# Kernel optimization log

Measured on AMD Instinct MI355X. Metric: run time of the kernel, lower is better.

Reference implementation:

```python
import jax, jax.numpy as jnp
from jax import lax
import numpy as np

V = 4096                 # variants per batch
NUM_READ_FEATURES = 24
NUM_INFO_FEATURES = 10
REF_LEN = 25             # ref sequence length (one-hot over ACGT)
CONV_C = 32
KERN = 3
READ_E = 128
INFO_E = 64
SEQ_E = 64
EMB = READ_E + INFO_E + SEQ_E   # 256, matches hstack of read/info/seq embeddings
FFN = 512                # self_attention_hidden_dimension
NUM_BLOCKS = 2           # num_self_attention_layers
AGG_H = 256
AGG_OUT = 128
WEIGHT_RANGE = 0.2


def _init_params(key):
    ks = iter(jax.random.split(key, 40))
    def lin(din, dout):
        w = jax.random.normal(next(ks), (din, dout), jnp.float32) / np.float32(np.sqrt(din))
        return w, jnp.zeros((dout,), jnp.float32)
    p = {}
    p['read_w1'], p['read_b1'] = lin(NUM_READ_FEATURES, READ_E)
    p['read_w2'], p['read_b2'] = lin(READ_E, READ_E)
    p['info_w1'], p['info_b1'] = lin(NUM_INFO_FEATURES, INFO_E)
    p['info_w2'], p['info_b2'] = lin(INFO_E, INFO_E)
    p['conv_w'] = jax.random.normal(next(ks), (CONV_C, 4, KERN), jnp.float32) / np.float32(np.sqrt(4 * KERN))
    p['conv_b'] = jnp.zeros((CONV_C,), jnp.float32)
    flat = CONV_C * (REF_LEN - KERN + 1)
    p['seq_w'], p['seq_b'] = lin(flat, SEQ_E)
    p['blk_w1'] = jax.random.normal(next(ks), (NUM_BLOCKS, EMB, FFN), jnp.float32) / np.float32(np.sqrt(EMB))
    p['blk_b1'] = jnp.zeros((NUM_BLOCKS, FFN), jnp.float32)
    p['blk_wg'] = jax.random.normal(next(ks), (NUM_BLOCKS, EMB, FFN), jnp.float32) / np.float32(np.sqrt(EMB))
    p['blk_bg'] = jnp.zeros((NUM_BLOCKS, FFN), jnp.float32)
    p['blk_w2'] = jax.random.normal(next(ks), (NUM_BLOCKS, FFN, EMB), jnp.float32) / np.float32(np.sqrt(FFN))
    p['blk_b2'] = jnp.zeros((NUM_BLOCKS, EMB), jnp.float32)
    p['agg_w1'], p['agg_b1'] = lin(EMB, AGG_H)
    p['agg_w2'], p['agg_b2'] = lin(AGG_H, AGG_OUT)
    return p


def setup_inputs() -> dict:
    rng = np.random.default_rng(0)
    ref_counts_np = rng.integers(5, 45, size=V)
    alt_counts_np = rng.integers(2, 23, size=V)
    total_ref = int(ref_counts_np.sum())
    total_alt = int(alt_counts_np.sum())
    key = jax.random.key(0)
    k1, k2, k3, kp = jax.random.split(key, 4)
    reads_2d = jax.random.normal(k1, (total_ref + total_alt, NUM_READ_FEATURES), jnp.float32)
    info_2d = jax.random.normal(k2, (V, NUM_INFO_FEATURES), jnp.float32)
    base_idx = rng.integers(0, 4, size=(V, REF_LEN))
    ref_seq_oh = jnp.asarray(np.eye(4, dtype=np.float32)[base_idx].transpose(0, 2, 1))  # [V,4,L]
    alt_u = jax.random.uniform(k3, (total_alt,), jnp.float32)  # replaces torch.rand for alt weights
    inp = {
        'reads_2d': reads_2d, 'info_2d': info_2d, 'ref_seq_oh': ref_seq_oh, 'alt_u': alt_u,
        'ref_counts': jnp.asarray(ref_counts_np, jnp.int32),
        'alt_counts': jnp.asarray(alt_counts_np, jnp.int32),
    }
    inp.update(_init_params(kp))
    return inp


def _mlp2(x, w1, b1, w2, b2):
    return jax.nn.relu(x @ w1 + b1) @ w2 + b2


def _forward(reads_2d, info_2d, ref_seq_oh, alt_u,
             read_w1, read_b1, read_w2, read_b2,
             info_w1, info_b1, info_w2, info_b2,
             conv_w, conv_b, seq_w, seq_b,
             blk_w1, blk_b1, blk_wg, blk_bg, blk_w2, blk_b2,
             agg_w1, agg_b1, agg_w2, agg_b2,
             ref_counts, alt_counts):
    total_alt = alt_u.shape[0]
    total_ref = reads_2d.shape[0] - total_alt
    # per-read and per-variant embeddings
    read_re = _mlp2(reads_2d, read_w1, read_b1, read_w2, read_b2)          # [R, READ_E]
    info_ve = _mlp2(info_2d, info_w1, info_b1, info_w2, info_b2)           # [V, INFO_E]
    conv = lax.conv_general_dilated(ref_seq_oh, conv_w, window_strides=(1,), padding='VALID',
                                    dimension_numbers=('NCH', 'OIH', 'NCH'))
    conv = jax.nn.relu(conv + conv_b[None, :, None])                       # [V, C, L-K+1]
    seq_ve = conv.reshape(conv.shape[0], -1) @ seq_w + seq_b               # [V, SEQ_E]
    info_seq_ve = jnp.concatenate([info_ve, seq_ve], axis=1)               # [V, INFO_E+SEQ_E]
    # ragged broadcast: variant-level rows repeated per read (repeat_interleave)
    ref_ids = jnp.repeat(jnp.arange(V), ref_counts, total_repeat_length=total_ref)
    alt_ids = jnp.repeat(jnp.arange(V), alt_counts, total_repeat_length=total_alt)
    ref_x = jnp.concatenate([read_re[:total_ref], info_seq_ve[ref_ids]], axis=1)   # [total_ref, EMB]
    alt_x = jnp.concatenate([read_re[total_ref:], info_seq_ve[alt_ids]], axis=1)   # [total_alt, EMB]
    ref_cf = ref_counts.astype(ref_x.dtype)[:, None]
    alt_cf = alt_counts.astype(alt_x.dtype)[:, None]
    # gated ref/alt encoder: per-read MLP cross-gated by the other set's segment mean
    for i in range(NUM_BLOCKS):
        ref_mean = jax.ops.segment_sum(ref_x, ref_ids, num_segments=V) / ref_cf
        alt_mean = jax.ops.segment_sum(alt_x, alt_ids, num_segments=V) / alt_cf
        def blk(x, gate_src):
            h = jax.nn.relu(x @ blk_w1[i] + blk_b1[i]) * jax.nn.sigmoid(gate_src @ blk_wg[i] + blk_bg[i])
            return h @ blk_w2[i] + blk_b2[i]
        ref_x = ref_x + blk(ref_x, alt_mean[ref_ids])
        alt_x = alt_x + blk(alt_x, ref_mean[alt_ids])
    # normalized weighted segment sums over alt reads (utils.sums_over_rows)
    w_r = 1.0 + WEIGHT_RANGE * (1.0 - 2.0 * alt_u)                          # [total_alt]
    wt_sums_v = jax.ops.segment_sum(w_r, alt_ids, num_segments=V)           # [V]
    norm_w = w_r / wt_sums_v[alt_ids]
    alt_means_ve = jax.ops.segment_sum(alt_x * norm_w[:, None], alt_ids, num_segments=V)  # [V, EMB]
    return _mlp2(alt_means_ve, agg_w1, agg_b1, agg_w2, agg_b2)              # [V, AGG_OUT]


def reference(reads_2d, info_2d, ref_seq_oh, alt_u,
              read_w1, read_b1, read_w2, read_b2,
              info_w1, info_b1, info_w2, info_b2,
              conv_w, conv_b, seq_w, seq_b,
              blk_w1, blk_b1, blk_wg, blk_bg, blk_w2, blk_b2,
              agg_w1, agg_b1, agg_w2, agg_b2,
              ref_counts, alt_counts):
    return _forward(reads_2d, info_2d, ref_seq_oh, alt_u,
                    read_w1, read_b1, read_w2, read_b2,
                    info_w1, info_b1, info_w2, info_b2,
                    conv_w, conv_b, seq_w, seq_b,
                    blk_w1, blk_b1, blk_wg, blk_bg, blk_w2, blk_b2,
                    agg_w1, agg_b1, agg_w2, agg_b2,
                    ref_counts, alt_counts)
```

## Files before the change

### kernel.cpp

```cpp
#include <hip/hip_runtime.h>
#include <math.h>


typedef short short8 __attribute__((ext_vector_type(8)));
typedef __bf16 bf16x8 __attribute__((ext_vector_type(8)));
typedef float f32x4 __attribute__((ext_vector_type(4)));

__device__ inline unsigned short f2bf(float f) {
    unsigned u = __builtin_bit_cast(unsigned, f);
    u += 0x7fffu + ((u >> 16) & 1u);
    return (unsigned short)(u >> 16);
}
__device__ inline float bf2f(unsigned short u) {
    unsigned v = ((unsigned)u) << 16;
    return __builtin_bit_cast(float, v);
}

__device__ inline f32x4 mfma16(short8 a, short8 b, f32x4 c) {
    return __builtin_amdgcn_mfma_f32_16x16x32_bf16(
        __builtin_bit_cast(bf16x8, a), __builtin_bit_cast(bf16x8, b), c, 0, 0, 0);
}

__device__ inline int lds_idx(int row, int k, int Kp, int mask) {
    return row * Kp + (k ^ ((row & mask) << 3));
}

__global__ __launch_bounds__(256) void scan_fill(
        const int* __restrict__ cref, const int* __restrict__ calt,
        int* __restrict__ off_r, int* __restrict__ off_a,
        int* __restrict__ rid_r, int* __restrict__ rid_a, int V) {
    __shared__ int part[256];
    const int* cnt = blockIdx.x ? calt : cref;
    int* off = blockIdx.x ? off_a : off_r;
    int* rid = blockIdx.x ? rid_a : rid_r;
    int t = threadIdx.x;
    int items = (V + 255) >> 8;
    int base = t * items;
    int s = 0;
    for (int i = 0; i < items; i++) {
        int idx = base + i;
        if (idx < V) s += cnt[idx];
    }
    part[t] = s;
    __syncthreads();
    for (int d = 1; d < 256; d <<= 1) {
        int v = (t >= d) ? part[t - d] : 0;
        __syncthreads();
        part[t] += v;
        __syncthreads();
    }
    int run = (t == 0) ? 0 : part[t - 1];
    for (int i = 0; i < items; i++) {
        int idx = base + i;
        if (idx < V) {
            off[idx] = run;
            run += cnt[idx];
        }
    }
    if (t == 255) off[V] = part[255];
    __syncthreads();
    for (int v = t; v < V; v += 256) {
        int s0 = off[v], e0 = off[v + 1];
        for (int r = s0; r < e0; r++) rid[r] = v;
    }
}

__device__ inline void pack_one(const float* __restrict__ src,
                                unsigned short* __restrict__ dst, int i,
                                int Ksrc, int K, int N, int ctN) {
    int e = i & 7;
    int lane = (i >> 3) & 63;
    int li = lane & 15, lg = lane >> 4;
    int r = i >> 9;
    int ct = r % ctN;
    int r2 = r / ctN;
    int sN = K >> 5;
    int s = r2 % sN;
    int strip = r2 / sN;
    int n = strip * (ctN << 4) + (ct << 4) + li;
    int k = (s << 5) + (lg << 3) + e;
    dst[i] = (k < Ksrc) ? f2bf(src[(size_t)k * N + n]) : (unsigned short)0;
}

__global__ __launch_bounds__(256) void pack_all(
        const float* __restrict__ w1, const float* __restrict__ wg,
        const float* __restrict__ w2, const float* __restrict__ rw1,
        const float* __restrict__ rw2, const float* __restrict__ ag1,
        const float* __restrict__ ag2,
        unsigned short* W1p0, unsigned short* W1p1,
        unsigned short* Wgp0, unsigned short* Wgp1,
        unsigned short* W2p0, unsigned short* W2p1,
        unsigned short* RW1p, unsigned short* RW2p,
        unsigned short* AG1p, unsigned short* AG2p) {
    int idx = blockIdx.x * 256 + threadIdx.x;
    if (idx < 131072)       pack_one(w1,          W1p0, idx,          256, 256, 512, 4);
    else if (idx < 262144)  pack_one(w1 + 131072, W1p1, idx - 131072, 256, 256, 512, 4);
    else if (idx < 393216)  pack_one(wg,          Wgp0, idx - 262144, 256, 256, 512, 4);
    else if (idx < 524288)  pack_one(wg + 131072, Wgp1, idx - 393216, 256, 256, 512, 4);
    else if (idx < 655360)  pack_one(w2,          W2p0, idx - 524288, 512, 512, 256, 2);
    else if (idx < 786432)  pack_one(w2 + 131072, W2p1, idx - 655360, 512, 512, 256, 2);
    else if (idx < 790528)  pack_one(rw1,         RW1p, idx - 786432, 24, 32, 128, 1);
    else if (idx < 806912)  pack_one(rw2,         RW2p, idx - 790528, 128, 128, 128, 1);
    else if (idx < 872448)  pack_one(ag1,         AG1p, idx - 806912, 256, 256, 256, 4);
    else if (idx < 905216)  pack_one(ag2,         AG2p, idx - 872448, 256, 256, 128, 4);
}

template <int EPI>
__global__ __launch_bounds__(256, 4) void gemm_bf16(
        const unsigned short* __restrict__ A, const unsigned short* __restrict__ Bp,
        const float* __restrict__ bias, void* __restrict__ C0,
        int M, int K, int mask, int ldc) {
    extern __shared__ unsigned short As[];
    const int m0 = blockIdx.x * 64, n0 = blockIdx.y * 64;
    const int tid = threadIdx.x;
    const int kc = K >> 3;
    for (int i = tid; i < (kc << 6); i += 256) {
        int r = i / kc, k8 = (i - r * kc) << 3;
        short8 v = {0, 0, 0, 0, 0, 0, 0, 0};
        if (m0 + r < M) v = *(const short8*)(A + (size_t)(m0 + r) * K + k8);
        *(short8*)&As[lds_idx(r, k8, K, mask)] = v;
    }
    __syncthreads();
    const int wid = tid >> 6, lane = tid & 63;
    const int lr = lane & 15, lg = lane >> 4;
    f32x4 acc[4];
#pragma unroll
    for (int ct = 0; ct < 4; ++ct) acc[ct] = f32x4{0.f, 0.f, 0.f, 0.f};
    const unsigned short* Bb = Bp + (size_t)blockIdx.y * ((size_t)K << 6) + (lane << 3);
    const int nk = K >> 5;
    for (int s = 0; s < nk; ++s) {
        int k0 = (s << 5) + (lg << 3);
        short8 af = *(const short8*)&As[lds_idx((wid << 4) + lr, k0, K, mask)];
#pragma unroll
        for (int ct = 0; ct < 4; ++ct) {
            short8 bf = *(const short8*)(Bb + (s << 11) + (ct << 9));
            acc[ct] = mfma16(af, bf, acc[ct]);
        }
    }
#pragma unroll
    for (int ct = 0; ct < 4; ++ct) {
        int c = n0 + (ct << 4) + lr;
        float bb = bias[c];
#pragma unroll
        for (int q = 0; q < 4; ++q) {
            int rg = m0 + (wid << 4) + (lg << 2) + q;
            if (rg >= M) continue;
            float v = acc[ct][q] + bb;
            if (EPI == 0) {
                ((float*)C0)[(size_t)rg * ldc + c] = v;
            } else if (EPI == 1) {
                ((unsigned short*)C0)[(size_t)rg * ldc + c] = f2bf(fmaxf(v, 0.f));
            } else {
                ((unsigned short*)C0)[(size_t)rg * ldc + c] = f2bf(1.f / (1.f + __expf(-v)));
            }
        }
    }
}

__global__ __launch_bounds__(512) void read_mlp_fused(
        const float* __restrict__ reads,
        const unsigned short* __restrict__ RW1p, const unsigned short* __restrict__ RW2p,
        const float* __restrict__ rb1, const float* __restrict__ rb2,
        const uint4* __restrict__ isv4,
        const int* __restrict__ rid_r, const int* __restrict__ rid_a,
        unsigned short* __restrict__ xref, unsigned short* __restrict__ xalt,
        int R, int TR) {
    __shared__ unsigned short Xs[64 * 32];
    __shared__ unsigned short Hs[64 * 128];
    __shared__ int rid_s[64];
    const int m0 = blockIdx.x * 64;
    const int tid = threadIdx.x;
    if (tid < 64) {
        int g = m0 + tid;
        rid_s[tid] = (g < R) ? (g < TR ? rid_r[g] : rid_a[g - TR]) : 0;
    }
    if (tid < 256) {
        int r = tid >> 2, c8 = (tid & 3) << 3;
        short8 v = {0, 0, 0, 0, 0, 0, 0, 0};
        int g = m0 + r;
        if (g < R && c8 < 24) {
            const float* sp = reads + (size_t)g * 24 + c8;
#pragma unroll
            for (int e = 0; e < 8; e++) v[e] = (short)f2bf(sp[e]);
        }
        *(short8*)&Xs[lds_idx(r, c8, 32, 3)] = v;
    }
    __syncthreads();
    const int wid = tid >> 6, lane = tid & 63;
    const int li = lane & 15, lg = lane >> 4;
    f32x4 a1[4];
#pragma unroll
    for (int rt = 0; rt < 4; ++rt) a1[rt] = f32x4{0.f, 0.f, 0.f, 0.f};
    short8 bw1 = *(const short8*)(RW1p + ((size_t)wid << 9) + (lane << 3));
#pragma unroll
    for (int rt = 0; rt < 4; ++rt) {
        short8 af = *(const short8*)&Xs[lds_idx(rt * 16 + li, lg << 3, 32, 3)];
        a1[rt] = mfma16(af, bw1, a1[rt]);
    }
    float b1v = rb1[(wid << 4) + li];
#pragma unroll
    for (int rt = 0; rt < 4; ++rt)
#pragma unroll
        for (int q = 0; q < 4; ++q) {
            int row = rt * 16 + (lg << 2) + q;
            Hs[lds_idx(row, (wid << 4) + li, 128, 15)] = f2bf(fmaxf(a1[rt][q] + b1v, 0.f));
        }
    __syncthreads();
    f32x4 a2[4];
#pragma unroll
    for (int rt = 0; rt < 4; ++rt) a2[rt] = f32x4{0.f, 0.f, 0.f, 0.f};
    const unsigned short* B2 = RW2p + ((size_t)wid << 11) + (lane << 3);
#pragma unroll
    for (int s = 0; s < 4; ++s) {
        short8 bw = *(const short8*)(B2 + (s << 9));
        int k0 = (s << 5) + (lg << 3);
#pragma unroll
        for (int rt = 0; rt < 4; ++rt) {
            short8 ah = *(const short8*)&Hs[lds_idx(rt * 16 + li, k0, 128, 15)];
            a2[rt] = mfma16(ah, bw, a2[rt]);
        }
    }
    float b2v = rb2[(wid << 4) + li];
    unsigned short ov[4][4];
#pragma unroll
    for (int rt = 0; rt < 4; ++rt)
#pragma unroll
        for (int q = 0; q < 4; ++q) ov[rt][q] = f2bf(a2[rt][q] + b2v);
    __syncthreads();
#pragma unroll
    for (int rt = 0; rt < 4; ++rt)
#pragma unroll
        for (int q = 0; q < 4; ++q) {
            int row = rt * 16 + (lg << 2) + q;
            Hs[row * 128 + (wid << 4) + li] = ov[rt][q];
        }
    __syncthreads();
#pragma unroll
    for (int u = 0; u < 4; ++u) {
        int i = tid + (u << 9);
        int r = i >> 5, j = i & 31;
        int g = m0 + r;
        if (g >= R) continue;
        unsigned short* dst = (g < TR) ? (xref + (size_t)g * 256)
                                       : (xalt + (size_t)(g - TR) * 256);
        if (j < 16)
            *(short8*)(dst + (j << 3)) = *(const short8*)&Hs[r * 128 + (j << 3)];
        else
            ((uint4*)(dst + 128))[j - 16] = isv4[(size_t)rid_s[r] * 16 + (j - 16)];
    }
}

__global__ __launch_bounds__(128) void variant_embed(
        const float* __restrict__ info2d, const float* __restrict__ oh,
        const float* __restrict__ iw1, const float* __restrict__ ib1,
        const float* __restrict__ iw2, const float* __restrict__ ib2,
        const float* __restrict__ cw, const float* __restrict__ cb,
        const float* __restrict__ sw, const float* __restrict__ sb,
        unsigned short* __restrict__ isv, int V) {
    __shared__ float iw1s[10 * 64], iw2s[64 * 64], ib1s[64], ib2s[64];
    __shared__ float cws[32 * 4 * 3], cbs[32];
    __shared__ float ohs[100], cv[736], his[64], infs[10];
    int v = blockIdx.x;
    int t = threadIdx.x;
    for (int i = t; i < 640; i += 128) iw1s[i] = iw1[i];
    for (int i = t; i < 4096; i += 128) iw2s[i] = iw2[i];
    for (int i = t; i < 384; i += 128) cws[i] = cw[i];
    if (t < 64) { ib1s[t] = ib1[t]; ib2s[t] = ib2[t]; }
    if (t < 32) cbs[t] = cb[t];
    for (int i = t; i < 100; i += 128) ohs[i] = oh[(size_t)v * 100 + i];
    if (t < 10) infs[t] = info2d[(size_t)v * 10 + t];
    __syncthreads();
    for (int j = t; j < 736; j += 128) {
        int c = j / 23, p = j - c * 23;
        float a = cbs[c];
#pragma unroll
        for (int i = 0; i < 4; i++)
#pragma unroll
            for (int k = 0; k < 3; k++)
                a += cws[(c * 4 + i) * 3 + k] * ohs[i * 25 + p + k];
        cv[j] = fmaxf(a, 0.f);
    }
    if (t < 64) {
        float h = ib1s[t];
#pragma unroll
        for (int k = 0; k < 10; k++) h += infs[k] * iw1s[k * 64 + t];
        his[t] = fmaxf(h, 0.f);
    }
    __syncthreads();
    if (t < 64) {
        float o = ib2s[t];
        for (int k = 0; k < 64; k++) o += his[k] * iw2s[k * 64 + t];
        isv[(size_t)v * 128 + t] = f2bf(o);
    } else {
        int tt = t - 64;
        float s = sb[tt];
        for (int j = 0; j < 736; j++) s += cv[j] * sw[j * 64 + tt];
        isv[(size_t)v * 128 + 64 + tt] = f2bf(s);
    }
}

__global__ __launch_bounds__(256) void seg_mean_bf(
        const unsigned short* __restrict__ xref, const int* __restrict__ off_r,
        const unsigned short* __restrict__ xalt, const int* __restrict__ off_a,
        unsigned short* __restrict__ m2, int V) {
    __shared__ float red[2048];
    int b = blockIdx.x;
    int t = threadIdx.x;
    const unsigned short* x;
    const int* off;
    unsigned short* out;
    int v;
    if (b < V) { x = xref; off = off_r; out = m2 + (size_t)(V + b) * 256; v = b; }
    else { x = xalt; off = off_a; out = m2 + (size_t)(b - V) * 256; v = b - V; }
    int s = off[v], e = off[v + 1];
    int g = t >> 5, c8 = (t & 31) << 3;
    float a[8] = {0.f, 0.f, 0.f, 0.f, 0.f, 0.f, 0.f, 0.f};
    for (int r = s + g; r < e; r += 8) {
        short8 vv = *(const short8*)(x + (size_t)r * 256 + c8);
#pragma unroll
        for (int k = 0; k < 8; k++) a[k] += bf2f((unsigned short)vv[k]);
    }
#pragma unroll
    for (int k = 0; k < 8; k++) red[g * 256 + c8 + k] = a[k];
    __syncthreads();
    float acc = red[t];
#pragma unroll
    for (int g2 = 1; g2 < 8; g2++) acc += red[g2 * 256 + t];
    out[t] = f2bf(acc / (float)(e - s));
}

__global__ __launch_bounds__(512, 4) void fused_block(
        unsigned short* __restrict__ xref, unsigned short* __restrict__ xalt,
        const unsigned short* __restrict__ W1p,
        const unsigned short* __restrict__ W2p,
        const float* __restrict__ b1, const float* __restrict__ b2,
        const unsigned short* __restrict__ gate_r, const unsigned short* __restrict__ gate_a,
        const int* __restrict__ rid_r, const int* __restrict__ rid_a,
        int TR, int TA, int ntr) {
    __shared__ unsigned short U[64 * 512];
    __shared__ int rid_s[64];
    const int nwg = gridDim.x;
    const int bid0 = blockIdx.x;
    const int q8 = nwg >> 3, r8 = nwg & 7;
    const int xcd = bid0 & 7;
    const int bid = (xcd < r8 ? xcd * (q8 + 1) : r8 * (q8 + 1) + (xcd - r8) * q8)
                    + (bid0 >> 3);
    const bool isref = bid < ntr;
    const int m0 = (isref ? bid : bid - ntr) * 64;
    const int M = isref ? TR : TA;
    unsigned short* x = isref ? xref : xalt;
    const unsigned short* gate = isref ? gate_r : gate_a;
    const int* rid = isref ? rid_r : rid_a;
    const int tid = threadIdx.x;
    if (tid < 64) rid_s[tid] = (m0 + tid < M) ? rid[m0 + tid] : 0;
#pragma unroll
    for (int u = 0; u < 4; ++u) {
        int i = tid + (u << 9);
        int r = i >> 5, j = i & 31;
        short8 v = {0, 0, 0, 0, 0, 0, 0, 0};
        if (m0 + r < M)
            v = *(const short8*)(x + (size_t)(m0 + r) * 256 + ((j ^ (r & 15)) << 3));
        *(short8*)&U[r * 256 + (j << 3)] = v;
    }
    __syncthreads();
    const int wid = tid >> 6, lane = tid & 63;
    const int li = lane & 15, lg = lane >> 4;
    const int ns = wid << 6;
    f32x4 acc1[4][4];
#pragma unroll
    for (int i = 0; i < 4; ++i)
#pragma unroll
        for (int j = 0; j < 4; ++j) acc1[i][j] = f32x4{0.f, 0.f, 0.f, 0.f};
    const unsigned short* W1b = W1p + ((size_t)wid << 14) + (lane << 3);
#pragma unroll
    for (int s = 0; s < 8; ++s) {
        short8 awc[4];
#pragma unroll
        for (int ct = 0; ct < 4; ++ct)
            awc[ct] = *(const short8*)(W1b + (s << 11) + (ct << 9));
        int k0 = (s << 5) + (lg << 3);
        __builtin_amdgcn_s_setprio(1);
#pragma unroll
        for (int rt = 0; rt < 4; ++rt) {
            short8 bx = *(const short8*)&U[lds_idx(rt * 16 + li, k0, 256, 15)];
#pragma unroll
            for (int ct = 0; ct < 4; ++ct)
                acc1[rt][ct] = mfma16(awc[ct], bx, acc1[rt][ct]);
        }
        __builtin_amdgcn_s_setprio(0);
    }
    __syncthreads();
#pragma unroll
    for (int rt = 0; rt < 4; ++rt) {
        int m = rt * 16 + li;
        const unsigned short* grow = gate + (size_t)rid_s[m] * 512 + ns + (lg << 2);
        const float* b1p = b1 + ns + (lg << 2);
#pragma unroll
        for (int ct = 0; ct < 4; ++ct) {
            uint2 gw = *(const uint2*)(grow + (ct << 4));
            float4 bv = *(const float4*)(b1p + (ct << 4));
            float g0 = bf2f((unsigned short)(gw.x & 0xffff));
            float g1 = bf2f((unsigned short)(gw.x >> 16));
            float g2 = bf2f((unsigned short)(gw.y & 0xffff));
            float g3 = bf2f((unsigned short)(gw.y >> 16));
            unsigned h0 = f2bf(fmaxf(acc1[rt][ct][0] + bv.x, 0.f) * g0);
            unsigned h1 = f2bf(fmaxf(acc1[rt][ct][1] + bv.y, 0.f) * g1);
            unsigned h2 = f2bf(fmaxf(acc1[rt][ct][2] + bv.z, 0.f) * g2);
            unsigned h3 = f2bf(fmaxf(acc1[rt][ct][3] + bv.w, 0.f) * g3);
            uint2 pk;
            pk.x = h0 | (h1 << 16);
            pk.y = h2 | (h3 << 16);
            int n = ns + (ct << 4) + (lg << 2);
            *(uint2*)&U[lds_idx(m, n, 512, 15)] = pk;
        }
    }
    __syncthreads();
    const int cs = wid << 5;
    f32x4 acc2[4][2];
#pragma unroll
    for (int i = 0; i < 4; ++i)
#pragma unroll
        for (int j = 0; j < 2; ++j) acc2[i][j] = f32x4{0.f, 0.f, 0.f, 0.f};
    const unsigned short* W2b = W2p + ((size_t)wid << 14) + (lane << 3);
    short8 bwc[2], bwn[2];
#pragma unroll
    for (int ct = 0; ct < 2; ++ct) bwc[ct] = *(const short8*)(W2b + (ct << 9));
#pragma unroll
    for (int s = 0; s < 16; ++s) {
        if (s < 15) {
#pragma unroll
            for (int ct = 0; ct < 2; ++ct)
                bwn[ct] = *(const short8*)(W2b + ((s + 1) << 10) + (ct << 9));
        }
        int k0 = (s << 5) + (lg << 3);
        __builtin_amdgcn_s_setprio(1);
#pragma unroll
        for (int rt = 0; rt < 4; ++rt) {
            short8 ah = *(const short8*)&U[lds_idx(rt * 16 + li, k0, 512, 15)];
#pragma unroll
            for (int ct = 0; ct < 2; ++ct)
                acc2[rt][ct] = mfma16(bwc[ct], ah, acc2[rt][ct]);
        }
        __builtin_amdgcn_s_setprio(0);
#pragma unroll
        for (int ct = 0; ct < 2; ++ct) bwc[ct] = bwn[ct];
    }
#pragma unroll
    for (int rt = 0; rt < 4; ++rt) {
        int m = rt * 16 + li;
        if (m0 + m >= M) continue;
        unsigned short* xrow = x + (size_t)(m0 + m) * 256;
#pragma unroll
        for (int ct = 0; ct < 2; ++ct) {
            int c = cs + (ct << 4) + (lg << 2);
            uint2 xv = *(const uint2*)(xrow + c);
            float4 bb = *(const float4*)(b2 + c);
            unsigned o0 = f2bf(bf2f((unsigned short)(xv.x & 0xffff)) + acc2[rt][ct][0] + bb.x);
            unsigned o1 = f2bf(bf2f((unsigned short)(xv.x >> 16)) + acc2[rt][ct][1] + bb.y);
            unsigned o2 = f2bf(bf2f((unsigned short)(xv.y & 0xffff)) + acc2[rt][ct][2] + bb.z);
            unsigned o3 = f2bf(bf2f((unsigned short)(xv.y >> 16)) + acc2[rt][ct][3] + bb.w);
            uint2 pk;
            pk.x = o0 | (o1 << 16);
            pk.y = o2 | (o3 << 16);
            *(uint2*)(xrow + c) = pk;
        }
    }
}

__global__ __launch_bounds__(256) void alt_weighted_mean_bf(
        const unsigned short* __restrict__ xalt, const float* __restrict__ au,
        const int* __restrict__ off_a, unsigned short* __restrict__ av, int V) {
    __shared__ float red[2048];
    __shared__ float wred[256];
    int v = blockIdx.x;
    int t = threadIdx.x;
    int s = off_a[v], e = off_a[v + 1];
    float wp = 0.f;
    for (int r = s + t; r < e; r += 256) wp += 1.2f - 0.4f * au[r];
    wred[t] = wp;
    __syncthreads();
    for (int d = 128; d; d >>= 1) {
        if (t < d) wred[t] += wred[t + d];
        __syncthreads();
    }
    float inv = 1.f / wred[0];
    int g = t >> 5, c8 = (t & 31) << 3;
    float a[8] = {0.f, 0.f, 0.f, 0.f, 0.f, 0.f, 0.f, 0.f};
    for (int r = s + g; r < e; r += 8) {
        float w = (1.2f - 0.4f * au[r]) * inv;
        short8 vv = *(const short8*)(xalt + (size_t)r * 256 + c8);
#pragma unroll
        for (int k = 0; k < 8; k++) a[k] += bf2f((unsigned short)vv[k]) * w;
    }
#pragma unroll
    for (int k = 0; k < 8; k++) red[g * 256 + c8 + k] = a[k];
    __syncthreads();
    float acc = red[t];
#pragma unroll
    for (int g2 = 1; g2 < 8; g2++) acc += red[g2 * 256 + t];
    av[(size_t)v * 256 + t] = f2bf(acc);
}

extern "C" void kernel_launch(void* const* d_in, const int* in_sizes, int n_in,
                              void* d_out, int out_size, void* d_ws, size_t ws_size,
                              hipStream_t stream) {
    const float* reads = (const float*)d_in[0];
    const float* info2d = (const float*)d_in[1];
    const float* oh = (const float*)d_in[2];
    const float* au = (const float*)d_in[3];
    const int* ref_counts = (const int*)d_in[4];
    const int* alt_counts = (const int*)d_in[5];
    const float* rw1 = (const float*)d_in[6];
    const float* rb1 = (const float*)d_in[7];
    const float* rw2 = (const float*)d_in[8];
    const float* rb2 = (const float*)d_in[9];
    const float* iw1 = (const float*)d_in[10];
    const float* ib1 = (const float*)d_in[11];
    const float* iw2 = (const float*)d_in[12];
    const float* ib2 = (const float*)d_in[13];
    const float* cw = (const float*)d_in[14];
    const float* cb = (const float*)d_in[15];
    const float* sw = (const float*)d_in[16];
    const float* sb = (const float*)d_in[17];
    const float* blk_w1 = (const float*)d_in[18];
    const float* blk_b1 = (const float*)d_in[19];
    const float* blk_wg = (const float*)d_in[20];
    const float* blk_bg = (const float*)d_in[21];
    const float* blk_w2 = (const float*)d_in[22];
    const float* blk_b2 = (const float*)d_in[23];
    const float* agg_w1 = (const float*)d_in[24];
    const float* agg_b1 = (const float*)d_in[25];
    const float* agg_w2 = (const float*)d_in[26];
    const float* agg_b2 = (const float*)d_in[27];

    const int R = in_sizes[0] / 24;
    const int TA = in_sizes[3];
    const int TR = R - TA;
    const int V = in_sizes[4];

    size_t p = 0;
    auto carve = [&](size_t bytes) -> void* {
        void* q = (char*)d_ws + p;
        p = (p + bytes + 255) & ~(size_t)255;
        return q;
    };
    int* off_r = (int*)carve((V + 1) * sizeof(int));
    int* off_a = (int*)carve((V + 1) * sizeof(int));
    int* rid_r = (int*)carve((size_t)TR * sizeof(int));
    int* rid_a = (int*)carve((size_t)TA * sizeof(int));
    unsigned short* isv = (unsigned short*)carve((size_t)V * 128 * 2);
    unsigned short* xref = (unsigned short*)carve((size_t)TR * 256 * 2);
    unsigned short* xalt = (unsigned short*)carve((size_t)TA * 256 * 2);
    unsigned short* W1p0 = (unsigned short*)carve((size_t)512 * 256 * 2);
    unsigned short* W1p1 = (unsigned short*)carve((size_t)512 * 256 * 2);
    unsigned short* Wgp0 = (unsigned short*)carve((size_t)512 * 256 * 2);
    unsigned short* Wgp1 = (unsigned short*)carve((size_t)512 * 256 * 2);
    unsigned short* W2p0 = (unsigned short*)carve((size_t)256 * 512 * 2);
    unsigned short* W2p1 = (unsigned short*)carve((size_t)256 * 512 * 2);
    unsigned short* RW1p = (unsigned short*)carve((size_t)128 * 32 * 2);
    unsigned short* RW2p = (unsigned short*)carve((size_t)128 * 128 * 2);
    unsigned short* AG1p = (unsigned short*)carve((size_t)256 * 256 * 2);
    unsigned short* AG2p = (unsigned short*)carve((size_t)128 * 256 * 2);
    unsigned short* m2 = (unsigned short*)carve((size_t)2 * V * 256 * 2);
    unsigned short* gate2 = (unsigned short*)carve((size_t)2 * V * 512 * 2);
    unsigned short* avb_bf = (unsigned short*)carve((size_t)V * 256 * 2);
    unsigned short* aggh_bf = (unsigned short*)carve((size_t)V * 256 * 2);
    (void)ws_size; (void)n_in; (void)out_size;

    scan_fill<<<2, 256, 0, stream>>>(ref_counts, alt_counts, off_r, off_a, rid_r, rid_a, V);
    pack_all<<<3536, 256, 0, stream>>>(blk_w1, blk_wg, blk_w2, rw1, rw2, agg_w1, agg_w2,
                                       W1p0, W1p1, Wgp0, Wgp1, W2p0, W2p1,
                                       RW1p, RW2p, AG1p, AG2p);
    variant_embed<<<V, 128, 0, stream>>>(info2d, oh, iw1, ib1, iw2, ib2, cw, cb, sw, sb, isv, V);

    read_mlp_fused<<<(R + 63) / 64, 512, 0, stream>>>(
        reads, RW1p, RW2p, rb1, rb2, (const uint4*)isv, rid_r, rid_a, xref, xalt, R, TR);

    const int ntr = (TR + 63) / 64, nta = (TA + 63) / 64;
    for (int it = 0; it < 2; ++it) {
        const unsigned short* W1p = it ? W1p1 : W1p0;
        const unsigned short* Wgp = it ? Wgp1 : Wgp0;
        const unsigned short* W2p = it ? W2p1 : W2p0;
        const float* B1 = blk_b1 + (size_t)it * 512;
        const float* Bg = blk_bg + (size_t)it * 512;
        const float* B2 = blk_b2 + (size_t)it * 256;

        seg_mean_bf<<<2 * V, 256, 0, stream>>>(xref, off_r, xalt, off_a, m2, V);
        dim3 gg(2 * V / 64, 8);
        gemm_bf16<2><<<gg, 256, 64 * 256 * 2, stream>>>(m2, Wgp, Bg, gate2,
                                                        2 * V, 256, 15, 512);
        fused_block<<<ntr + nta, 512, 0, stream>>>(xref, xalt, W1p, W2p, B1, B2,
                                                   gate2, gate2 + (size_t)V * 512,
                                                   rid_r, rid_a, TR, TA, ntr);
    }

    alt_weighted_mean_bf<<<V, 256, 0, stream>>>(xalt, au, off_a, avb_bf, V);
    {
        dim3 ga(V / 64, 4);
        gemm_bf16<1><<<ga, 256, 64 * 256 * 2, stream>>>(avb_bf, AG1p, agg_b1, aggh_bf,
                                                        V, 256, 15, 256);
        dim3 go(V / 64, 2);
        gemm_bf16<0><<<go, 256, 64 * 256 * 2, stream>>>(aggh_bf, AG2p, agg_b2, d_out,
                                                        V, 256, 15, 128);
    }
}
```

Measured before the change: 450.1 us.

## Batch eight variants per block in variant embedding and drop setprio hints

The variant embedding kernel now handles eight variants per 256-thread block. Each 64-row tile of the seq_w matrix is staged through shared memory and reused across the eight variants, instead of every variant's block reading the full 736x64 weight matrix from global memory. Conv activations are stored as bf16 in LDS to fit, which slightly changes numerics. Separately, the setprio hints around the MFMA loops are removed and f2bf now uses the compiler's native bf16 conversion. V must be a multiple of 8.

New measurement: 955.0 us. +112.2%, slower.

```diff
diff --git a/kernel.cpp b/kernel.cpp
--- a/kernel.cpp
+++ b/kernel.cpp
@@ -7,9 +7,7 @@
 typedef float f32x4 __attribute__((ext_vector_type(4)));
 
 __device__ inline unsigned short f2bf(float f) {
-    unsigned u = __builtin_bit_cast(unsigned, f);
-    u += 0x7fffu + ((u >> 16) & 1u);
-    return (unsigned short)(u >> 16);
+    return __builtin_bit_cast(unsigned short, (__bf16)f);
 }
 __device__ inline float bf2f(unsigned short u) {
     unsigned v = ((unsigned)u) << 16;
@@ -250,53 +248,69 @@
     }
 }
 
-__global__ __launch_bounds__(128) void variant_embed(
+__global__ __launch_bounds__(256) void variant_embed8(
         const float* __restrict__ info2d, const float* __restrict__ oh,
         const float* __restrict__ iw1, const float* __restrict__ ib1,
         const float* __restrict__ iw2, const float* __restrict__ ib2,
         const float* __restrict__ cw, const float* __restrict__ cb,
         const float* __restrict__ sw, const float* __restrict__ sb,
         unsigned short* __restrict__ isv, int V) {
-    __shared__ float iw1s[10 * 64], iw2s[64 * 64], ib1s[64], ib2s[64];
-    __shared__ float cws[32 * 4 * 3], cbs[32];
-    __shared__ float ohs[100], cv[736], his[64], infs[10];
-    int v = blockIdx.x;
-    int t = threadIdx.x;
-    for (int i = t; i < 640; i += 128) iw1s[i] = iw1[i];
-    for (int i = t; i < 4096; i += 128) iw2s[i] = iw2[i];
-    for (int i = t; i < 384; i += 128) cws[i] = cw[i];
-    if (t < 64) { ib1s[t] = ib1[t]; ib2s[t] = ib2[t]; }
+    __shared__ float iw1s[640], iw2s[4096], ib1s[64], ib2s[64];
+    __shared__ float cws[384], cbs[32], sbs[64];
+    __shared__ float ohs[800], infs[80], his[512];
+    __shared__ unsigned short cvs[8 * 736];
+    __shared__ float swt[4096];
+    const int v0 = blockIdx.x * 8;
+    const int t = threadIdx.x;
+    for (int i = t; i < 640; i += 256) iw1s[i] = iw1[i];
+    for (int i = t; i < 4096; i += 256) iw2s[i] = iw2[i];
+    for (int i = t; i < 384; i += 256) cws[i] = cw[i];
+    if (t < 64) { ib1s[t] = ib1[t]; ib2s[t] = ib2[t]; sbs[t] = sb[t]; }
     if (t < 32) cbs[t] = cb[t];
-    for (int i = t; i < 100; i += 128) ohs[i] = oh[(size_t)v * 100 + i];
-    if (t < 10) infs[t] = info2d[(size_t)v * 10 + t];
-    __syncthreads();
-    for (int j = t; j < 736; j += 128) {
-        int c = j / 23, p = j - c * 23;
+    for (int i = t; i < 800; i += 256) ohs[i] = oh[(size_t)v0 * 100 + i];
+    if (t < 80) infs[t] = info2d[(size_t)v0 * 10 + t];
+    __syncthreads();
+    for (int g = t; g < 8 * 736; g += 256) {
+        int v = g / 736, j = g - v * 736;
+        int c = j / 23, pp = j - c * 23;
         float a = cbs[c];
 #pragma unroll
         for (int i = 0; i < 4; i++)
 #pragma unroll
             for (int k = 0; k < 3; k++)
-                a += cws[(c * 4 + i) * 3 + k] * ohs[i * 25 + p + k];
-        cv[j] = fmaxf(a, 0.f);
-    }
-    if (t < 64) {
-        float h = ib1s[t];
-#pragma unroll
-        for (int k = 0; k < 10; k++) h += infs[k] * iw1s[k * 64 + t];
-        his[t] = fmaxf(h, 0.f);
-    }
-    __syncthreads();
-    if (t < 64) {
-        float o = ib2s[t];
-        for (int k = 0; k < 64; k++) o += his[k] * iw2s[k * 64 + t];
-        isv[(size_t)v * 128 + t] = f2bf(o);
-    } else {
-        int tt = t - 64;
-        float s = sb[tt];
-        for (int j = 0; j < 736; j++) s += cv[j] * sw[j * 64 + tt];
-        isv[(size_t)v * 128 + 64 + tt] = f2bf(s);
-    }
+                a += cws[(c * 4 + i) * 3 + k] * ohs[v * 100 + i * 25 + pp + k];
+        cvs[g] = f2bf(fmaxf(a, 0.f));
+    }
+    for (int g = t; g < 512; g += 256) {
+        int v = g >> 6, tt = g & 63;
+        float h = ib1s[tt];
+#pragma unroll
+        for (int k = 0; k < 10; k++) h += infs[v * 10 + k] * iw1s[k * 64 + tt];
+        his[g] = fmaxf(h, 0.f);
+    }
+    __syncthreads();
+    for (int g = t; g < 512; g += 256) {
+        int v = g >> 6, tt = g & 63;
+        float o = ib2s[tt];
+        for (int k = 0; k < 64; k++) o += his[v * 64 + k] * iw2s[k * 64 + tt];
+        isv[(size_t)(v0 + v) * 128 + tt] = f2bf(o);
+    }
+    const int tt = t & 63;
+    const int va = t >> 6, vb = 4 + (t >> 6);
+    float acc0 = 0.f, acc1 = 0.f;
+    for (int j0 = 0; j0 < 736; j0 += 64) {
+        int len = min(64, 736 - j0);
+        __syncthreads();
+        for (int l = t; l < len * 64; l += 256) swt[l] = sw[(size_t)j0 * 64 + l];
+        __syncthreads();
+        for (int jj = 0; jj < len; jj++) {
+            float w = swt[jj * 64 + tt];
+            acc0 += bf2f(cvs[va * 736 + j0 + jj]) * w;
+            acc1 += bf2f(cvs[vb * 736 + j0 + jj]) * w;
+        }
+    }
+    isv[(size_t)(v0 + va) * 128 + 64 + tt] = f2bf(acc0 + sbs[tt]);
+    isv[(size_t)(v0 + vb) * 128 + 64 + tt] = f2bf(acc1 + sbs[tt]);
 }
 
 __global__ __launch_bounds__(256) void seg_mean_bf(
@@ -379,7 +393,6 @@
         for (int ct = 0; ct < 4; ++ct)
             awc[ct] = *(const short8*)(W1b + (s << 11) + (ct << 9));
         int k0 = (s << 5) + (lg << 3);
-        __builtin_amdgcn_s_setprio(1);
 #pragma unroll
         for (int rt = 0; rt < 4; ++rt) {
             short8 bx = *(const short8*)&U[lds_idx(rt * 16 + li, k0, 256, 15)];
@@ -387,7 +400,6 @@
             for (int ct = 0; ct < 4; ++ct)
                 acc1[rt][ct] = mfma16(awc[ct], bx, acc1[rt][ct]);
         }
-        __builtin_amdgcn_s_setprio(0);
     }
     __syncthreads();
 #pragma unroll
@@ -433,7 +445,6 @@
                 bwn[ct] = *(const short8*)(W2b + ((s + 1) << 10) + (ct << 9));
         }
         int k0 = (s << 5) + (lg << 3);
-        __builtin_amdgcn_s_setprio(1);
 #pragma unroll
         for (int rt = 0; rt < 4; ++rt) {
             short8 ah = *(const short8*)&U[lds_idx(rt * 16 + li, k0, 512, 15)];
@@ -441,7 +452,6 @@
             for (int ct = 0; ct < 2; ++ct)
                 acc2[rt][ct] = mfma16(bwc[ct], ah, acc2[rt][ct]);
         }
-        __builtin_amdgcn_s_setprio(0);
 #pragma unroll
         for (int ct = 0; ct < 2; ++ct) bwc[ct] = bwn[ct];
     }
@@ -571,7 +581,8 @@
     pack_all<<<3536, 256, 0, stream>>>(blk_w1, blk_wg, blk_w2, rw1, rw2, agg_w1, agg_w2,
                                        W1p0, W1p1, Wgp0, Wgp1, W2p0, W2p1,
                                        RW1p, RW2p, AG1p, AG2p);
-    variant_embed<<<V, 128, 0, stream>>>(info2d, oh, iw1, ib1, iw2, ib2, cw, cb, sw, sb, isv, V);
+    variant_embed8<<<V / 8, 256, 0, stream>>>(info2d, oh, iw1, ib1, iw2, ib2,
+                                              cw, cb, sw, sb, isv, V);
 
     read_mlp_fused<<<(R + 63) / 64, 512, 0, stream>>>(
         reads, RW1p, RW2p, rb1, rb2, (const uint4*)isv, rid_r, rid_a, xref, xalt, R, TR);
```
